# Performance work log

Hardware: AMD Instinct MI355X
Metric: run time of the kernel (lower is better)

Reference implementation:

```python
import jax, jax.numpy as jnp
import numpy as np

B, S, D, K = 32, 512, 512, 2048
NHEADS, NHASH, HLEN = 8, 4, 16
COMMIT = 0.25


def _conv1d(x, w, b):
    # x: [B, C, S], w: [O, I, k] (torch Conv1d layout), 'same' padding for odd k
    k = w.shape[-1]
    y = jax.lax.conv_general_dilated(x, w, (1,), [(k // 2, k // 2)],
                                     dimension_numbers=('NCH', 'OIH', 'NCH'))
    return y + b[None, :, None]


def _mha(x, in_w, in_b, out_w, out_b, nheads):
    # torch nn.MultiheadAttention (batch_first) with packed in_proj
    b, s, d = x.shape
    dh = d // nheads
    qkv = x @ in_w.T + in_b
    q, k, v = jnp.split(qkv, 3, axis=-1)
    sp = lambda t: t.reshape(b, s, nheads, dh).transpose(0, 2, 1, 3)
    q, k, v = sp(q), sp(k), sp(v)
    attn = jax.nn.softmax(jnp.einsum('bhqd,bhkd->bhqk', q, k) * (dh ** -0.5), axis=-1)
    o = jnp.einsum('bhqk,bhkd->bhqd', attn, v).transpose(0, 2, 1, 3).reshape(b, s, d)
    return o @ out_w.T + out_b


def setup_inputs() -> dict:
    key = jax.random.key(0)
    ks = jax.random.split(key, 16)
    w = lambda k, shape, s=0.02: jax.random.normal(k, shape, jnp.float32) * s
    z = lambda *shape: jnp.zeros(shape, jnp.float32)
    return {
        'market_data': jax.random.normal(ks[0], (B, S, D), jnp.float32),
        'W_in': w(ks[1], (D, D)), 'b_in': z(D),
        'pos_enc': w(ks[2], (S, D)),
        'conv3_w': w(ks[3], (D, D, 3)), 'conv3_b': z(D),
        'conv5_w': w(ks[4], (D, D, 5)), 'conv5_b': z(D),
        'conv7_w': w(ks[5], (D, D, 7)), 'conv7_b': z(D),
        'conv9_w': w(ks[6], (D, D, 9)), 'conv9_b': z(D),
        'ms_proj_w': w(ks[7], (D, 4 * D)), 'ms_proj_b': z(D),
        'in_proj_w': w(ks[8], (3 * D, D)), 'in_proj_b': z(3 * D),
        'attn_out_w': w(ks[9], (D, D)), 'attn_out_b': z(D),
        'codebook': jax.random.uniform(ks[10], (K, D), jnp.float32, -1.0 / K, 1.0 / K),
        'hash_w': w(ks[11], (NHASH, HLEN, D), 1.0),
        'reg1_w': w(ks[12], (D // 2, D)), 'reg1_b': z(D // 2),
        'reg2_w': w(ks[13], (K, D // 2)), 'reg2_b': z(K),
    }


def reference(market_data, W_in, b_in, pos_enc, conv3_w, conv3_b, conv5_w, conv5_b,
              conv7_w, conv7_b, conv9_w, conv9_b, ms_proj_w, ms_proj_b,
              in_proj_w, in_proj_b, attn_out_w, attn_out_b, codebook, hash_w,
              reg1_w, reg1_b, reg2_w, reg2_b):
    # input projection
    x = market_data @ W_in.T + b_in                                   # [B,S,D]
    # --- subsequence encoder ---
    xp = x + pos_enc[:x.shape[1]][None]
    xt = xp.transpose(0, 2, 1)                                        # [B,D,S]
    scales = [jax.nn.relu(_conv1d(xt, cw, cb)).transpose(0, 2, 1)
              for cw, cb in ((conv3_w, conv3_b), (conv5_w, conv5_b),
                             (conv7_w, conv7_b), (conv9_w, conv9_b))]
    multi = jnp.concatenate(scales, axis=-1)                          # [B,S,4D]
    proj = multi @ ms_proj_w.T + ms_proj_b                            # [B,S,D]
    enc = proj + _mha(proj, in_proj_w, in_proj_b, attn_out_w, attn_out_b, NHEADS)
    # --- vector quantizer (eval mode: no EMA update) ---
    flat = enc.reshape(-1, D)                                         # [N,D]
    dist = (jnp.sum(flat * flat, axis=1, keepdims=True)
            + jnp.sum(codebook * codebook, axis=1)
            - 2.0 * (flat @ codebook.T))                              # [N,K]
    idx = jnp.argmin(dist, axis=1)                                    # [N]
    quant = codebook[idx].reshape(enc.shape)
    commit = jnp.mean((jax.lax.stop_gradient(quant) - enc) ** 2)
    cb_loss = jnp.mean((quant - jax.lax.stop_gradient(enc)) ** 2)
    vq_loss = COMMIT * commit + cb_loss
    quant_st = enc + jax.lax.stop_gradient(quant - enc)               # straight-through
    # --- hash encoder on semantic ids ---
    hash_codes = (jnp.einsum('bsd,nhd->bsnh', quant_st, hash_w) > 0).astype(jnp.float32)
    # --- regime classifier ---
    h = jax.nn.relu(quant_st @ reg1_w.T + reg1_b)
    regime = jax.nn.softmax(h @ reg2_w.T + reg2_b, axis=-1)
    return (quant_st, vq_loss, idx.reshape(enc.shape[:-1]), hash_codes, regime)
```

## Files before the change

kernel.cpp:

```cpp
#include <hip/hip_runtime.h>
#include <hip/hip_bf16.h>


#define GF_BIAS 1
#define GF_RELU 2
#define GF_ADD  4
#define GF_POS  8
#define GF_ACC  16

typedef _Float16 f16x8 __attribute__((ext_vector_type(8)));
typedef float    f32x4 __attribute__((ext_vector_type(4)));

static constexpr long long O_QUANT = 0LL;
static constexpr long long O_LOSS  = 8388608LL;
static constexpr long long O_IDX   = 8388609LL;
static constexpr long long O_HASH  = 8404993LL;
static constexpr long long O_REG   = 9453569LL;
static constexpr long long O_END   = 43008001LL;

static constexpr long long W_XP    = 0LL;
static constexpr long long W_CT    = 8388608LL;
static constexpr long long W_PROJ  = 16777216LL;
static constexpr long long W_VW    = 25165824LL;
static constexpr long long W_HREG  = 33554432LL;
static constexpr long long W_T     = 34078720LL;
static constexpr long long W_IDX   = 34209792LL;
static constexpr long long W_ASUM  = 34226176LL;
static constexpr long long W_CBB   = 34258944LL;
static constexpr long long W_LPART = 34263040LL;
static constexpr long long W_PBV   = 34271232LL;
static constexpr long long W_PBI   = 34336768LL;
static constexpr long long W_END   = 34402304LL;

__device__ __forceinline__ unsigned int pack_hl(float x)
{
    _Float16 h = (_Float16)x;
    float hf = (float)h;
    _Float16 l = (_Float16)(x - hf);
    unsigned short hb = __builtin_bit_cast(unsigned short, h);
    unsigned short lb = __builtin_bit_cast(unsigned short, l);
    return (unsigned int)hb | ((unsigned int)lb << 16);
}

__device__ __forceinline__ void split2(float x, unsigned short& h, unsigned short& l)
{
    _Float16 hf = (_Float16)x;
    _Float16 lf = (_Float16)(x - (float)hf);
    h = __builtin_bit_cast(unsigned short, hf);
    l = __builtin_bit_cast(unsigned short, lf);
}

__global__ __launch_bounds__(256)
void split_xp_r18(float* __restrict__ xp)
{
    long long i = (long long)blockIdx.x*256 + threadIdx.x;
    float x = xp[i];
    ((unsigned int*)xp)[i] = pack_hl(x);
}

template<int KT>
__global__ __launch_bounds__(256)
void conv_w_tr_r18(const float* __restrict__ w, unsigned int* __restrict__ wt)
{
    long long i = (long long)blockIdx.x*256 + threadIdx.x;
    int o  = (int)(i / (512*KT));
    int rem= (int)(i % (512*KT));
    int t  = rem >> 9;
    int ii = rem & 511;
    wt[i] = pack_hl(w[(long long)o*512*KT + (long long)ii*KT + t]);
}

template<int KT>
__global__ __launch_bounds__(256)
void conv_mfma_r18(const unsigned int* __restrict__ xphl,
                   const unsigned int* __restrict__ wthl,
                   const float* __restrict__ bias, float* __restrict__ outp)
{
    constexpr int PAD = KT / 2;
    __shared__ unsigned short Ah[128][56];
    __shared__ unsigned short Al[128][56];
    __shared__ unsigned short Bh[128][56];
    __shared__ unsigned short Bl[128][56];
    const int tid  = threadIdx.x;
    const int lane = tid & 63;
    const int wave = tid >> 6;
    const int wm = (wave >> 1) * 64, wn = (wave & 1) * 64;
    const int bm = blockIdx.x * 128, bn = blockIdx.y * 128;
    const int l15 = lane & 15;
    const int lk8 = (lane >> 4) * 8;
    const int rbase = (lane >> 4) * 4;
    const int cg   = tid & 7;
    const int rw0  = tid >> 3;

    f32x4 acc[4][4];
    #pragma unroll
    for (int i=0;i<4;i++)
        #pragma unroll
        for (int j=0;j<4;j++)
            acc[i][j] = (f32x4){0.f,0.f,0.f,0.f};

    for (int t = 0; t < KT; ++t) {
        for (int i0 = 0; i0 < 512; i0 += 32) {
            uint4 va[4], vb[4];
            #pragma unroll
            for (int q = 0; q < 4; ++q) {
                const int row = rw0 + q*32;
                const int s   = (bm + row) & 511;
                const int sp  = s + t - PAD;
                if (sp >= 0 && sp < 512)
                    va[q] = *(const uint4*)(xphl + (long long)(bm + row + t - PAD)*512 + i0 + cg*4);
                else
                    va[q] = make_uint4(0u,0u,0u,0u);
                vb[q] = *(const uint4*)(wthl + (long long)(bn + row)*(KT*512) + t*512 + i0 + cg*4);
            }
            __syncthreads();
            #pragma unroll
            for (int q = 0; q < 4; ++q) {
                const int row = rw0 + q*32;
                ushort4 ahi = make_ushort4((unsigned short)(va[q].x & 0xffff),
                                           (unsigned short)(va[q].y & 0xffff),
                                           (unsigned short)(va[q].z & 0xffff),
                                           (unsigned short)(va[q].w & 0xffff));
                ushort4 alo = make_ushort4((unsigned short)(va[q].x >> 16),
                                           (unsigned short)(va[q].y >> 16),
                                           (unsigned short)(va[q].z >> 16),
                                           (unsigned short)(va[q].w >> 16));
                ushort4 bhi = make_ushort4((unsigned short)(vb[q].x & 0xffff),
                                           (unsigned short)(vb[q].y & 0xffff),
                                           (unsigned short)(vb[q].z & 0xffff),
                                           (unsigned short)(vb[q].w & 0xffff));
                ushort4 blo = make_ushort4((unsigned short)(vb[q].x >> 16),
                                           (unsigned short)(vb[q].y >> 16),
                                           (unsigned short)(vb[q].z >> 16),
                                           (unsigned short)(vb[q].w >> 16));
                *(ushort4*)(&Ah[row][cg*4]) = ahi;
                *(ushort4*)(&Al[row][cg*4]) = alo;
                *(ushort4*)(&Bh[row][cg*4]) = bhi;
                *(ushort4*)(&Bl[row][cg*4]) = blo;
            }
            __syncthreads();
            f16x8 ah[4], al[4], bh[4], bl[4];
            #pragma unroll
            for (int mi = 0; mi < 4; ++mi) {
                ah[mi] = *(const f16x8*)(&Ah[wm + mi*16 + l15][lk8]);
                al[mi] = *(const f16x8*)(&Al[wm + mi*16 + l15][lk8]);
            }
            #pragma unroll
            for (int nj = 0; nj < 4; ++nj) {
                bh[nj] = *(const f16x8*)(&Bh[wn + nj*16 + l15][lk8]);
                bl[nj] = *(const f16x8*)(&Bl[wn + nj*16 + l15][lk8]);
            }
            #pragma unroll
            for (int mi = 0; mi < 4; ++mi)
                #pragma unroll
                for (int nj = 0; nj < 4; ++nj) {
                    acc[mi][nj] = __builtin_amdgcn_mfma_f32_16x16x32_f16(ah[mi], bh[nj], acc[mi][nj], 0, 0, 0);
                    acc[mi][nj] = __builtin_amdgcn_mfma_f32_16x16x32_f16(ah[mi], bl[nj], acc[mi][nj], 0, 0, 0);
                    acc[mi][nj] = __builtin_amdgcn_mfma_f32_16x16x32_f16(al[mi], bh[nj], acc[mi][nj], 0, 0, 0);
                }
        }
    }
    #pragma unroll
    for (int mi = 0; mi < 4; ++mi) {
        #pragma unroll
        for (int nj = 0; nj < 4; ++nj) {
            const int col = bn + wn + nj*16 + l15;
            const float bcol = bias[col];
            #pragma unroll
            for (int r = 0; r < 4; ++r) {
                const int row = bm + wm + mi*16 + rbase + r;
                float v = acc[mi][nj][r] + bcol;
                outp[(long long)row*512 + col] = fmaxf(v, 0.0f);
            }
        }
    }
}

template<int FLAGS>
__global__ __launch_bounds__(256)
void gemm_mfma_r18(const float* __restrict__ A, const float* __restrict__ Bm,
                   const float* __restrict__ bias, const float* __restrict__ pos,
                   const float* __restrict__ addsrc, float* __restrict__ C,
                   int Kdim, int lda, int ldb, int ldc)
{
    __shared__ unsigned short Ah[128][56];
    __shared__ unsigned short Al[128][56];
    __shared__ unsigned short Bh[128][56];
    __shared__ unsigned short Bl[128][56];
    const int tid  = threadIdx.x;
    const int lane = tid & 63;
    const int wave = tid >> 6;
    const int wm = (wave >> 1) * 64, wn = (wave & 1) * 64;
    const int bm = blockIdx.x * 128, bn = blockIdx.y * 128;
    const int l15 = lane & 15;
    const int lk8 = (lane >> 4) * 8;
    const int rbase = (lane >> 4) * 4;
    const int cg   = tid & 7;
    const int rw0  = tid >> 3;

    f32x4 acc[4][4];
    #pragma unroll
    for (int i=0;i<4;i++)
        #pragma unroll
        for (int j=0;j<4;j++)
            acc[i][j] = (f32x4){0.f,0.f,0.f,0.f};

    for (int k0 = 0; k0 < Kdim; k0 += 32) {
        float4 fa[4], fb[4];
        #pragma unroll
        for (int q = 0; q < 4; ++q) {
            const int row = rw0 + q*32;
            fa[q] = *(const float4*)(A  + (long long)(bm + row)*lda + k0 + cg*4);
            fb[q] = *(const float4*)(Bm + (long long)(bn + row)*ldb + k0 + cg*4);
        }
        __syncthreads();
        #pragma unroll
        for (int q = 0; q < 4; ++q) {
            const int row = rw0 + q*32;
            ushort4 ah_, al_, bh_, bl_;
            split2(fa[q].x, ah_.x, al_.x);
            split2(fa[q].y, ah_.y, al_.y);
            split2(fa[q].z, ah_.z, al_.z);
            split2(fa[q].w, ah_.w, al_.w);
            split2(fb[q].x, bh_.x, bl_.x);
            split2(fb[q].y, bh_.y, bl_.y);
            split2(fb[q].z, bh_.z, bl_.z);
            split2(fb[q].w, bh_.w, bl_.w);
            *(ushort4*)(&Ah[row][cg*4]) = ah_;
            *(ushort4*)(&Al[row][cg*4]) = al_;
            *(ushort4*)(&Bh[row][cg*4]) = bh_;
            *(ushort4*)(&Bl[row][cg*4]) = bl_;
        }
        __syncthreads();
        f16x8 ah[4], al[4], bh[4], bl[4];
        #pragma unroll
        for (int mi = 0; mi < 4; ++mi) {
            ah[mi] = *(const f16x8*)(&Ah[wm + mi*16 + l15][lk8]);
            al[mi] = *(const f16x8*)(&Al[wm + mi*16 + l15][lk8]);
        }
        #pragma unroll
        for (int nj = 0; nj < 4; ++nj) {
            bh[nj] = *(const f16x8*)(&Bh[wn + nj*16 + l15][lk8]);
            bl[nj] = *(const f16x8*)(&Bl[wn + nj*16 + l15][lk8]);
        }
        #pragma unroll
        for (int mi = 0; mi < 4; ++mi)
            #pragma unroll
            for (int nj = 0; nj < 4; ++nj) {
                acc[mi][nj] = __builtin_amdgcn_mfma_f32_16x16x32_f16(ah[mi], bh[nj], acc[mi][nj], 0, 0, 0);
                acc[mi][nj] = __builtin_amdgcn_mfma_f32_16x16x32_f16(ah[mi], bl[nj], acc[mi][nj], 0, 0, 0);
                acc[mi][nj] = __builtin_amdgcn_mfma_f32_16x16x32_f16(al[mi], bh[nj], acc[mi][nj], 0, 0, 0);
            }
    }
    #pragma unroll
    for (int mi = 0; mi < 4; ++mi) {
        #pragma unroll
        for (int nj = 0; nj < 4; ++nj) {
            const int col = bn + wn + nj*16 + l15;
            #pragma unroll
            for (int r = 0; r < 4; ++r) {
                const int row = bm + wm + mi*16 + rbase + r;
                float v = acc[mi][nj][r];
                if constexpr (FLAGS & GF_BIAS) v += bias[col];
                if constexpr (FLAGS & GF_POS)  v += pos[(long long)(row & 511)*512 + col];
                if constexpr (FLAGS & GF_ADD)  v += addsrc[(long long)row*ldc + col];
                if constexpr (FLAGS & GF_ACC)  v += C[(long long)row*ldc + col];
                if constexpr (FLAGS & GF_RELU) v = fmaxf(v, 0.0f);
                C[(long long)row*ldc + col] = v;
            }
        }
    }
}

__global__ __launch_bounds__(256)
void attn_mfma_r18(const float* __restrict__ Qbuf, const float* __restrict__ Kbuf,
                   const float* __restrict__ Vbuf, float* __restrict__ att)
{
    __shared__ unsigned short Qh[64][68];
    __shared__ unsigned short Ql[64][68];
    __shared__ unsigned short Kh[64][68];
    __shared__ unsigned short Kl[64][68];
    __shared__ unsigned short Vh[64][68];
    __shared__ unsigned short Vl[64][68];
    const int tid  = threadIdx.x;
    const int lane = tid & 63;
    const int wave = tid >> 6;
    const int l15  = lane & 15;
    const int lq   = lane >> 4;
    const int lq8  = lq * 8;
    const int bid = blockIdx.x;
    const int qt = bid & 7, h = (bid >> 3) & 7, b = bid >> 6;
    const int row0 = b*512 + qt*64;

    #pragma unroll
    for (int u = 0; u < 16; ++u) {
        int e = u*256 + tid;
        int r = e >> 6, c = e & 63;
        float q = Qbuf[(long long)(row0 + r)*512 + h*64 + c] * 0.125f;
        unsigned short hs, ls;
        split2(q, hs, ls);
        Qh[r][c] = hs; Ql[r][c] = ls;
    }

    float m[4], l[4];
    f32x4 accO[4];
    #pragma unroll
    for (int r=0;r<4;r++){ m[r] = -1e30f; l[r] = 0.f; }
    #pragma unroll
    for (int j=0;j<4;j++) accO[j] = (f32x4){0.f,0.f,0.f,0.f};

    for (int kv = 0; kv < 512; kv += 64) {
        __syncthreads();
        #pragma unroll
        for (int u = 0; u < 16; ++u) {
            int e = u*256 + tid;
            int r = e >> 6, c = e & 63;
            float kvf = Kbuf[(long long)(b*512 + kv + r)*512 + h*64 + c];
            float vvf = Vbuf[(long long)(b*512 + kv + r)*512 + h*64 + c];
            unsigned short hs, ls;
            split2(kvf, hs, ls);
            Kh[r][c] = hs; Kl[r][c] = ls;
            split2(vvf, hs, ls);
            Vh[c][r] = hs; Vl[c][r] = ls;
        }
        __syncthreads();
        f32x4 accS[4];
        #pragma unroll
        for (int j=0;j<4;j++) accS[j] = (f32x4){0.f,0.f,0.f,0.f};
        #pragma unroll
        for (int ks = 0; ks < 2; ++ks) {
            f16x8 qh = *(const f16x8*)(&Qh[wave*16 + l15][ks*32 + lq8]);
            f16x8 ql = *(const f16x8*)(&Ql[wave*16 + l15][ks*32 + lq8]);
            #pragma unroll
            for (int nj = 0; nj < 4; ++nj) {
                f16x8 kh = *(const f16x8*)(&Kh[nj*16 + l15][ks*32 + lq8]);
                f16x8 kl = *(const f16x8*)(&Kl[nj*16 + l15][ks*32 + lq8]);
                accS[nj] = __builtin_amdgcn_mfma_f32_16x16x32_f16(qh, kh, accS[nj], 0, 0, 0);
                accS[nj] = __builtin_amdgcn_mfma_f32_16x16x32_f16(qh, kl, accS[nj], 0, 0, 0);
                accS[nj] = __builtin_amdgcn_mfma_f32_16x16x32_f16(ql, kh, accS[nj], 0, 0, 0);
            }
        }
        #pragma unroll
        for (int r = 0; r < 4; ++r) {
            float tm = fmaxf(fmaxf(accS[0][r], accS[1][r]), fmaxf(accS[2][r], accS[3][r]));
            #pragma unroll
            for (int msk = 1; msk < 16; msk <<= 1) tm = fmaxf(tm, __shfl_xor(tm, msk, 64));
            float mn = fmaxf(m[r], tm);
            float scale = expf(m[r] - mn);
            float rs = 0.f;
            #pragma unroll
            for (int nj = 0; nj < 4; ++nj) {
                float p = expf(accS[nj][r] - mn);
                accS[nj][r] = p;
                rs += p;
            }
            #pragma unroll
            for (int msk = 1; msk < 16; msk <<= 1) rs += __shfl_xor(rs, msk, 64);
            l[r] = l[r]*scale + rs;
            m[r] = mn;
            #pragma unroll
            for (int nj = 0; nj < 4; ++nj) accO[nj][r] *= scale;
        }
        __syncthreads();
        #pragma unroll
        for (int r = 0; r < 4; ++r)
            #pragma unroll
            for (int nj = 0; nj < 4; ++nj) {
                unsigned short hs, ls;
                split2(accS[nj][r], hs, ls);
                Kh[wave*16 + lq*4 + r][nj*16 + l15] = hs;
                Kl[wave*16 + lq*4 + r][nj*16 + l15] = ls;
            }
        __syncthreads();
        #pragma unroll
        for (int ks = 0; ks < 2; ++ks) {
            f16x8 ph = *(const f16x8*)(&Kh[wave*16 + l15][ks*32 + lq8]);
            f16x8 pl = *(const f16x8*)(&Kl[wave*16 + l15][ks*32 + lq8]);
            #pragma unroll
            for (int nj = 0; nj < 4; ++nj) {
                f16x8 vh = *(const f16x8*)(&Vh[nj*16 + l15][ks*32 + lq8]);
                f16x8 vl = *(const f16x8*)(&Vl[nj*16 + l15][ks*32 + lq8]);
                accO[nj] = __builtin_amdgcn_mfma_f32_16x16x32_f16(ph, vh, accO[nj], 0, 0, 0);
                accO[nj] = __builtin_amdgcn_mfma_f32_16x16x32_f16(ph, vl, accO[nj], 0, 0, 0);
                accO[nj] = __builtin_amdgcn_mfma_f32_16x16x32_f16(pl, vh, accO[nj], 0, 0, 0);
            }
        }
    }
    #pragma unroll
    for (int nj = 0; nj < 4; ++nj)
        #pragma unroll
        for (int r = 0; r < 4; ++r) {
            const int row = row0 + wave*16 + lq*4 + r;
            att[(long long)row*512 + h*64 + nj*16 + l15] = accO[nj][r] / l[r];
        }
}

__global__ __launch_bounds__(256)
void row_sumsq_r18(const float* __restrict__ X, double* __restrict__ outp)
{
    const int row  = blockIdx.x*4 + (threadIdx.x >> 6);
    const int lane = threadIdx.x & 63;
    double s = 0.0;
    #pragma unroll
    for (int u = 0; u < 8; ++u) {
        float v = X[(long long)row*512 + lane + u*64];
        s += (double)v * (double)v;
    }
    #pragma unroll
    for (int msk = 32; msk; msk >>= 1) s += __shfl_xor(s, msk, 64);
    if (lane == 0) outp[row] = s;
}

__global__ __launch_bounds__(256)
void vq_argmin_mfma_r18(const float* __restrict__ enc, const float* __restrict__ cb,
                        const double* __restrict__ Asum, const double* __restrict__ cbB,
                        float* __restrict__ pbv, int* __restrict__ pbi)
{
    __shared__ unsigned int smem[14336];
    unsigned short* AhP = (unsigned short*)smem;
    unsigned short* AlP = AhP + 128*56;
    unsigned short* BhP = AlP + 128*56;
    unsigned short* BlP = BhP + 128*56;
    float* bvsP = (float*)smem;
    int*   bisP = (int*)(smem + 4096);

    const int tid  = threadIdx.x;
    const int lane = tid & 63;
    const int wave = tid >> 6;
    const int wm = (wave >> 1) * 64, wn = (wave & 1) * 64;
    const int bm = blockIdx.x * 128;
    const int l15 = lane & 15;
    const int lk8 = (lane >> 4) * 8;
    const int rbase = (lane >> 4) * 4;
    const int cg   = tid & 7;
    const int rw0  = tid >> 3;

    float bestv[16]; int besti[16];
    #pragma unroll
    for (int g = 0; g < 16; ++g) { bestv[g] = 3.0e38f; besti[g] = 2048; }

    for (int nb = 0; nb < 4; ++nb) {
        const int ct0 = blockIdx.y * 512 + nb * 128;
        f32x4 acc[4][4];
        #pragma unroll
        for (int i=0;i<4;i++)
            #pragma unroll
            for (int j=0;j<4;j++)
                acc[i][j] = (f32x4){0.f,0.f,0.f,0.f};

        for (int k0 = 0; k0 < 512; k0 += 32) {
            float4 fa[4], fb[4];
            #pragma unroll
            for (int q = 0; q < 4; ++q) {
                const int row = rw0 + q*32;
                fa[q] = *(const float4*)(enc + (long long)(bm + row)*512 + k0 + cg*4);
                fb[q] = *(const float4*)(cb  + (long long)(ct0 + row)*512 + k0 + cg*4);
            }
            __syncthreads();
            #pragma unroll
            for (int q = 0; q < 4; ++q) {
                const int row = rw0 + q*32;
                ushort4 ah_, al_, bh_, bl_;
                split2(fa[q].x, ah_.x, al_.x);
                split2(fa[q].y, ah_.y, al_.y);
                split2(fa[q].z, ah_.z, al_.z);
                split2(fa[q].w, ah_.w, al_.w);
                split2(fb[q].x * 2048.0f, bh_.x, bl_.x);
                split2(fb[q].y * 2048.0f, bh_.y, bl_.y);
                split2(fb[q].z * 2048.0f, bh_.z, bl_.z);
                split2(fb[q].w * 2048.0f, bh_.w, bl_.w);
                *(ushort4*)(&AhP[row*56 + cg*4]) = ah_;
                *(ushort4*)(&AlP[row*56 + cg*4]) = al_;
                *(ushort4*)(&BhP[row*56 + cg*4]) = bh_;
                *(ushort4*)(&BlP[row*56 + cg*4]) = bl_;
            }
            __syncthreads();
            f16x8 ah[4], al[4], bh[4], bl[4];
            #pragma unroll
            for (int mi = 0; mi < 4; ++mi) {
                ah[mi] = *(const f16x8*)(&AhP[(wm + mi*16 + l15)*56 + lk8]);
                al[mi] = *(const f16x8*)(&AlP[(wm + mi*16 + l15)*56 + lk8]);
            }
            #pragma unroll
            for (int nj = 0; nj < 4; ++nj) {
                bh[nj] = *(const f16x8*)(&BhP[(wn + nj*16 + l15)*56 + lk8]);
                bl[nj] = *(const f16x8*)(&BlP[(wn + nj*16 + l15)*56 + lk8]);
            }
            #pragma unroll
            for (int mi = 0; mi < 4; ++mi)
                #pragma unroll
                for (int nj = 0; nj < 4; ++nj) {
                    acc[mi][nj] = __builtin_amdgcn_mfma_f32_16x16x32_f16(ah[mi], bh[nj], acc[mi][nj], 0, 0, 0);
                    acc[mi][nj] = __builtin_amdgcn_mfma_f32_16x16x32_f16(ah[mi], bl[nj], acc[mi][nj], 0, 0, 0);
                    acc[mi][nj] = __builtin_amdgcn_mfma_f32_16x16x32_f16(al[mi], bh[nj], acc[mi][nj], 0, 0, 0);
                }
        }
        #pragma unroll
        for (int mi = 0; mi < 4; ++mi) {
            #pragma unroll
            for (int r = 0; r < 4; ++r) {
                const int g = mi*4 + r;
                const float anf = (float)Asum[bm + wm + mi*16 + rbase + r];
                #pragma unroll
                for (int nj = 0; nj < 4; ++nj) {
                    const int col = ct0 + wn + nj*16 + l15;
                    const float bf = (float)cbB[col];
                    const float s1 = anf + bf;
                    const float dot = acc[mi][nj][r] * (1.0f/2048.0f);
                    const float df  = 2.0f * dot;
                    const float qd  = s1 - df;
                    if (qd < bestv[g] || (qd == bestv[g] && col < besti[g])) {
                        bestv[g] = qd; besti[g] = col;
                    }
                }
            }
        }
    }
    __syncthreads();
    #pragma unroll
    for (int mi = 0; mi < 4; ++mi)
        #pragma unroll
        for (int r = 0; r < 4; ++r) {
            const int row  = wm + mi*16 + rbase + r;
            const int slot = (wave & 1)*16 + l15;
            bvsP[row*32 + slot] = bestv[mi*4 + r];
            bisP[row*32 + slot] = besti[mi*4 + r];
        }
    __syncthreads();
    if (tid < 128) {
        float bv = bvsP[tid*32]; int bi = bisP[tid*32];
        #pragma unroll
        for (int s = 1; s < 32; ++s) {
            float v = bvsP[tid*32 + s]; int ii = bisP[tid*32 + s];
            if (v < bv || (v == bv && ii < bi)) { bv = v; bi = ii; }
        }
        pbv[(long long)blockIdx.y*16384 + bm + tid] = bv;
        pbi[(long long)blockIdx.y*16384 + bm + tid] = bi;
    }
}

__global__ __launch_bounds__(256)
void vq_reduce_r18(const float* __restrict__ pbv, const int* __restrict__ pbi,
                   int* __restrict__ idxout)
{
    int n = blockIdx.x*256 + threadIdx.x;
    if (n >= 16384) return;
    float bv = pbv[n]; int bi = pbi[n];
    #pragma unroll
    for (int q = 1; q < 4; ++q) {
        float v = pbv[q*16384 + n]; int ii = pbi[q*16384 + n];
        if (v < bv || (v == bv && ii < bi)) { bv = v; bi = ii; }
    }
    idxout[n] = bi & 2047;
}

__global__ __launch_bounds__(256)
void vq_loss_partial_r18(const float* __restrict__ enc, const float* __restrict__ cb,
                         const int* __restrict__ idxp, double* __restrict__ part)
{
    __shared__ double red[4];
    const int row  = blockIdx.x*4 + (threadIdx.x >> 6);
    const int lane = threadIdx.x & 63;
    const int ci = idxp[row] & 2047;
    double s = 0.0;
    #pragma unroll
    for (int u = 0; u < 8; ++u) {
        int d = lane + u*64;
        double dv = (double)cb[(long long)ci*512 + d] - (double)enc[(long long)row*512 + d];
        s += dv * dv;
    }
    #pragma unroll
    for (int msk = 32; msk; msk >>= 1) s += __shfl_xor(s, msk, 64);
    if (lane == 0) red[threadIdx.x >> 6] = s;
    __syncthreads();
    if (threadIdx.x == 0)
        part[blockIdx.x] = red[0] + red[1] + red[2] + red[3];
}

template<int FLAGS>
__global__ __launch_bounds__(256)
void gemm_bt_r18(const float* __restrict__ A, const float* __restrict__ Bm,
                 const float* __restrict__ bias, const float* __restrict__ pos,
                 const float* __restrict__ addsrc, float* __restrict__ C,
                 int Kdim, int lda, int ldb, int ldc)
{
    __shared__ float As[16][132];
    __shared__ float Bs[16][132];
    const int tid = threadIdx.x;
    const int tx = tid & 15, ty = tid >> 4;
    const int bm = blockIdx.x * 128, bn = blockIdx.y * 128;
    const int r0 = tid >> 2;
    const int kg = (tid & 3) << 2;
    const float* Arow0 = A  + (long long)(bm + r0) * lda + kg;
    const float* Arow1 = A  + (long long)(bm + r0 + 64) * lda + kg;
    const float* Brow0 = Bm + (long long)(bn + r0) * ldb + kg;
    const float* Brow1 = Bm + (long long)(bn + r0 + 64) * ldb + kg;

    float acc[8][8] = {};
    for (int k0 = 0; k0 < Kdim; k0 += 16) {
        float4 a0 = *(const float4*)(Arow0 + k0);
        float4 a1 = *(const float4*)(Arow1 + k0);
        float4 b0 = *(const float4*)(Brow0 + k0);
        float4 b1 = *(const float4*)(Brow1 + k0);
        __syncthreads();
        As[kg+0][r0]=a0.x; As[kg+1][r0]=a0.y; As[kg+2][r0]=a0.z; As[kg+3][r0]=a0.w;
        As[kg+0][r0+64]=a1.x; As[kg+1][r0+64]=a1.y; As[kg+2][r0+64]=a1.z; As[kg+3][r0+64]=a1.w;
        Bs[kg+0][r0]=b0.x; Bs[kg+1][r0]=b0.y; Bs[kg+2][r0]=b0.z; Bs[kg+3][r0]=b0.w;
        Bs[kg+0][r0+64]=b1.x; Bs[kg+1][r0+64]=b1.y; Bs[kg+2][r0+64]=b1.z; Bs[kg+3][r0+64]=b1.w;
        __syncthreads();
        #pragma unroll
        for (int kk = 0; kk < 16; ++kk) {
            float a[8], b[8];
            #pragma unroll
            for (int i=0;i<8;i++) a[i] = As[kk][ty*8+i];
            #pragma unroll
            for (int j=0;j<4;j++) b[j]   = Bs[kk][tx*4+j];
            #pragma unroll
            for (int j=0;j<4;j++) b[4+j] = Bs[kk][64+tx*4+j];
            #pragma unroll
            for (int i=0;i<8;i++)
                #pragma unroll
                for (int j=0;j<8;j++)
                    acc[i][j] = fmaf(a[i], b[j], acc[i][j]);
        }
    }
    #pragma unroll
    for (int i=0;i<8;i++){
        const int row = bm + ty*8 + i;
        #pragma unroll
        for (int j=0;j<8;j++){
            const int col = bn + ((j < 4) ? (tx*4 + j) : (64 + tx*4 + (j-4)));
            float v = acc[i][j];
            if constexpr (FLAGS & GF_BIAS) v += bias[col];
            if constexpr (FLAGS & GF_POS)  v += pos[(long long)(row & 511)*512 + col];
            if constexpr (FLAGS & GF_ADD)  v += addsrc[(long long)row*ldc + col];
            if constexpr (FLAGS & GF_ACC)  v += C[(long long)row*ldc + col];
            if constexpr (FLAGS & GF_RELU) v = fmaxf(v, 0.0f);
            C[(long long)row*ldc + col] = v;
        }
    }
}

__global__ __launch_bounds__(256)
void softmax_rows_r18(float* __restrict__ R)
{
    const int row = blockIdx.x;
    const int tid = threadIdx.x;
    __shared__ float  redf[256];
    __shared__ double redd[256];
    float* p = R + (long long)row * 2048;
    float mx = -1e30f;
    for (int c = tid; c < 2048; c += 256) mx = fmaxf(mx, p[c]);
    redf[tid] = mx; __syncthreads();
    for (int s2 = 128; s2; s2 >>= 1) { if (tid < s2) redf[tid] = fmaxf(redf[tid], redf[tid+s2]); __syncthreads(); }
    mx = redf[0];
    double sum = 0.0;
    for (int c = tid; c < 2048; c += 256) { float e = expf(p[c] - mx); p[c] = e; sum += e; }
    redd[tid] = sum; __syncthreads();
    for (int s2 = 128; s2; s2 >>= 1) { if (tid < s2) redd[tid] += redd[tid+s2]; __syncthreads(); }
    double tot = redd[0];
    for (int c = tid; c < 2048; c += 256) p[c] = (float)((double)p[c] / tot);
}

__global__ __launch_bounds__(256)
void hash_table_r18(const float* __restrict__ cb, const float* __restrict__ hw,
                    float* __restrict__ T)
{
    const int k = blockIdx.x*4 + (threadIdx.x >> 6);
    const int j = threadIdx.x & 63;
    double s = 0.0;
    for (int d = 0; d < 512; ++d)
        s += (double)cb[(long long)k*512 + d] * (double)hw[(long long)j*512 + d];
    T[(long long)k*64 + j] = (s > 0.0) ? 1.0f : 0.0f;
}

__global__ void write_loss_r18(const double* __restrict__ part,
                               float* __restrict__ out)
{
    __shared__ double red[256];
    double s = 0.0;
    for (int i = threadIdx.x; i < 4096; i += 256) s += part[i];
    red[threadIdx.x] = s; __syncthreads();
    for (int s2 = 128; s2; s2 >>= 1) {
        if (threadIdx.x < s2) red[threadIdx.x] += red[threadIdx.x + s2];
        __syncthreads();
    }
    if (threadIdx.x == 0)
        out[O_LOSS] = (float)(1.25 * red[0] / 8388608.0);
}

__global__ __launch_bounds__(256)
void write_regime_r18(const float* __restrict__ R, const int* __restrict__ idxp,
                      float* __restrict__ out)
{
    long long i = (long long)blockIdx.x*256 + threadIdx.x;
    if (i >= 33554432LL) return;
    int n = (int)(i >> 11), c = (int)(i & 2047);
    int ci = idxp[n] & 2047;
    out[O_REG + i] = R[(long long)ci*2048 + c];
}

__global__ __launch_bounds__(256)
void write_hash_r18(const float* __restrict__ T, const int* __restrict__ idxp,
                    float* __restrict__ out)
{
    long long i = (long long)blockIdx.x*256 + threadIdx.x;
    if (i >= 1048576LL) return;
    int n = (int)(i >> 6), j = (int)(i & 63);
    int ci = idxp[n] & 2047;
    out[O_HASH + i] = T[(long long)ci*64 + j];
}

__global__ __launch_bounds__(256)
void write_idx_r18(const int* __restrict__ idxp, float* __restrict__ out)
{
    int n = blockIdx.x*256 + threadIdx.x;
    if (n >= 16384) return;
    out[O_IDX + n] = (float)(idxp[n] & 2047);
}

__global__ __launch_bounds__(256)
void write_quant_r18(const float* __restrict__ cb, const int* __restrict__ idxp,
                     float* __restrict__ out)
{
    long long i = (long long)blockIdx.x*256 + threadIdx.x;
    if (i >= 8388608LL) return;
    int n = (int)(i >> 9), d = (int)(i & 511);
    int ci = idxp[n] & 2047;
    out[O_QUANT + i] = cb[(long long)ci*512 + d];
}

extern "C" void kernel_launch(void* const* d_in, const int* in_sizes, int n_in,
                              void* d_out, int out_size, void* d_ws, size_t ws_size,
                              hipStream_t stream)
{
    (void)in_sizes; (void)n_in; (void)out_size;
    const float* market = (const float*)d_in[0];
    const float* W_in   = (const float*)d_in[1];
    const float* b_in   = (const float*)d_in[2];
    const float* pos    = (const float*)d_in[3];
    const float* c3w = (const float*)d_in[4];  const float* c3b = (const float*)d_in[5];
    const float* c5w = (const float*)d_in[6];  const float* c5b = (const float*)d_in[7];
    const float* c7w = (const float*)d_in[8];  const float* c7b = (const float*)d_in[9];
    const float* c9w = (const float*)d_in[10]; const float* c9b = (const float*)d_in[11];
    const float* msw = (const float*)d_in[12]; const float* msb = (const float*)d_in[13];
    const float* inw = (const float*)d_in[14]; const float* inb = (const float*)d_in[15];
    const float* aow = (const float*)d_in[16]; const float* aob = (const float*)d_in[17];
    const float* cb  = (const float*)d_in[18]; const float* hw  = (const float*)d_in[19];
    const float* r1w = (const float*)d_in[20]; const float* r1b = (const float*)d_in[21];
    const float* r2w = (const float*)d_in[22]; const float* r2b = (const float*)d_in[23];

    if (ws_size < (size_t)W_END * sizeof(float)) return;

    float* ws    = (float*)d_ws;
    float* xp    = ws + W_XP;
    float* convt = ws + W_CT;
    float* projp = ws + W_PROJ;
    unsigned int* wt3 = (unsigned int*)(ws + W_VW);
    unsigned int* wt5 = wt3 + 512*512*3;
    unsigned int* wt7 = wt5 + 512*512*5;
    unsigned int* wt9 = wt7 + 512*512*7;
    float* Vbufp = ws + W_VW;
    float* hregp = ws + W_HREG;
    float* Tp    = ws + W_T;
    int*    idxp  = (int*)(ws + W_IDX);
    double* asump = (double*)(ws + W_ASUM);
    double* cbbp  = (double*)(ws + W_CBB);
    double* lpart = (double*)(ws + W_LPART);
    float*  pbvp  = ws + W_PBV;
    int*    pbip  = (int*)(ws + W_PBI);

    float* out = (float*)d_out;

    float* Qbufp = xp;
    float* attp  = xp;
    float* Kbufp = convt;
    float* encp  = convt;
    float* Rp    = projp;

    const unsigned int* xpu = (const unsigned int*)xp;

    conv_w_tr_r18<3><<<3072, 256, 0, stream>>>(c3w, wt3);
    conv_w_tr_r18<5><<<5120, 256, 0, stream>>>(c5w, wt5);
    conv_w_tr_r18<7><<<7168, 256, 0, stream>>>(c7w, wt7);
    conv_w_tr_r18<9><<<9216, 256, 0, stream>>>(c9w, wt9);

    const dim3 gT(128, 4);

    gemm_mfma_r18<GF_BIAS|GF_POS><<<gT, 256, 0, stream>>>(market, W_in, b_in, pos, nullptr, xp, 512, 512, 512, 512);
    split_xp_r18<<<32768, 256, 0, stream>>>(xp);

    conv_mfma_r18<3><<<gT, 256, 0, stream>>>(xpu, wt3, c3b, convt);
    gemm_mfma_r18<GF_BIAS><<<gT, 256, 0, stream>>>(convt, msw + 0*512, msb, nullptr, nullptr, projp, 512, 512, 2048, 512);
    conv_mfma_r18<5><<<gT, 256, 0, stream>>>(xpu, wt5, c5b, convt);
    gemm_mfma_r18<GF_ACC><<<gT, 256, 0, stream>>>(convt, msw + 1*512, nullptr, nullptr, nullptr, projp, 512, 512, 2048, 512);
    conv_mfma_r18<7><<<gT, 256, 0, stream>>>(xpu, wt7, c7b, convt);
    gemm_mfma_r18<GF_ACC><<<gT, 256, 0, stream>>>(convt, msw + 2*512, nullptr, nullptr, nullptr, projp, 512, 512, 2048, 512);
    conv_mfma_r18<9><<<gT, 256, 0, stream>>>(xpu, wt9, c9b, convt);
    gemm_mfma_r18<GF_ACC><<<gT, 256, 0, stream>>>(convt, msw + 3*512, nullptr, nullptr, nullptr, projp, 512, 512, 2048, 512);

    gemm_mfma_r18<GF_BIAS><<<gT, 256, 0, stream>>>(projp, inw + 512*512,  inb + 512,  nullptr, nullptr, Kbufp, 512, 512, 512, 512);
    gemm_mfma_r18<GF_BIAS><<<gT, 256, 0, stream>>>(projp, inw + 1024*512, inb + 1024, nullptr, nullptr, Vbufp, 512, 512, 512, 512);
    gemm_mfma_r18<GF_BIAS><<<gT, 256, 0, stream>>>(projp, inw,            inb,        nullptr, nullptr, Qbufp, 512, 512, 512, 512);

    attn_mfma_r18<<<2048, 256, 0, stream>>>(Qbufp, Kbufp, Vbufp, attp);

    gemm_mfma_r18<GF_BIAS|GF_ADD><<<gT, 256, 0, stream>>>(attp, aow, aob, nullptr, projp, encp, 512, 512, 512, 512);

    row_sumsq_r18<<<4096, 256, 0, stream>>>(encp, asump);
    row_sumsq_r18<<<512,  256, 0, stream>>>(cb, cbbp);
    vq_argmin_mfma_r18<<<dim3(128, 4), 256, 0, stream>>>(encp, cb, asump, cbbp, pbvp, pbip);
    vq_reduce_r18<<<64, 256, 0, stream>>>(pbvp, pbip, idxp);
    vq_loss_partial_r18<<<4096, 256, 0, stream>>>(encp, cb, idxp, lpart);

    gemm_bt_r18<GF_BIAS|GF_RELU><<<dim3(16, 2),  256, 0, stream>>>(cb, r1w, r1b, nullptr, nullptr, hregp, 512, 512, 512, 256);
    gemm_bt_r18<GF_BIAS><<<dim3(16, 16), 256, 0, stream>>>(hregp, r2w, r2b, nullptr, nullptr, Rp, 256, 256, 256, 2048);
    softmax_rows_r18<<<2048, 256, 0, stream>>>(Rp);
    hash_table_r18<<<512, 256, 0, stream>>>(cb, hw, Tp);

    write_loss_r18<<<1, 256, 0, stream>>>(lpart, out);
    write_regime_r18<<<131072, 256, 0, stream>>>(Rp, idxp, out);
    write_hash_r18<<<4096, 256, 0, stream>>>(Tp, idxp, out);
    write_idx_r18<<<64, 256, 0, stream>>>(idxp, out);
    write_quant_r18<<<32768, 256, 0, stream>>>(cb, idxp, out);
}
```

Baseline: 1.631 ms.

## Reuse haloed input tile across conv taps in MFMA conv kernel

The conv kernel now loops over input-channel chunks on the outside and taps on the inside. For each chunk it loads one 136-row input tile with a 4-row halo into shared memory, then reads it at a shifted row offset per tap instead of reloading the input once per tap. This cuts global reads of the activation by roughly the kernel width and reshapes the LDS tiles to 40-wide rows. In exchange, the weight stores to LDS become scalar 16-bit writes instead of vector writes, and an extra barrier is added per tap. The other kernels are only renamed.

```diff
diff --git a/kernel.cpp b/kernel.cpp
--- a/kernel.cpp
+++ b/kernel.cpp
@@ -51,7 +51,7 @@
 }
 
 __global__ __launch_bounds__(256)
-void split_xp_r18(float* __restrict__ xp)
+void split_xp_r19(float* __restrict__ xp)
 {
     long long i = (long long)blockIdx.x*256 + threadIdx.x;
     float x = xp[i];
@@ -60,7 +60,7 @@
 
 template<int KT>
 __global__ __launch_bounds__(256)
-void conv_w_tr_r18(const float* __restrict__ w, unsigned int* __restrict__ wt)
+void conv_w_tr_r19(const float* __restrict__ w, unsigned int* __restrict__ wt)
 {
     long long i = (long long)blockIdx.x*256 + threadIdx.x;
     int o  = (int)(i / (512*KT));
@@ -72,15 +72,15 @@
 
 template<int KT>
 __global__ __launch_bounds__(256)
-void conv_mfma_r18(const unsigned int* __restrict__ xphl,
+void conv_mfma_r19(const unsigned int* __restrict__ xphl,
                    const unsigned int* __restrict__ wthl,
                    const float* __restrict__ bias, float* __restrict__ outp)
 {
     constexpr int PAD = KT / 2;
-    __shared__ unsigned short Ah[128][56];
-    __shared__ unsigned short Al[128][56];
-    __shared__ unsigned short Bh[128][56];
-    __shared__ unsigned short Bl[128][56];
+    __shared__ unsigned short Ah[136][40];
+    __shared__ unsigned short Al[136][40];
+    __shared__ unsigned short Bh[128][40];
+    __shared__ unsigned short Bl[128][40];
     const int tid  = threadIdx.x;
     const int lane = tid & 63;
     const int wave = tid >> 6;
@@ -89,8 +89,7 @@
     const int l15 = lane & 15;
     const int lk8 = (lane >> 4) * 8;
     const int rbase = (lane >> 4) * 4;
-    const int cg   = tid & 7;
-    const int rw0  = tid >> 3;
+    const int sb = bm & 511;
 
     f32x4 acc[4][4];
     #pragma unroll
@@ -99,51 +98,43 @@
         for (int j=0;j<4;j++)
             acc[i][j] = (f32x4){0.f,0.f,0.f,0.f};
 
-    for (int t = 0; t < KT; ++t) {
-        for (int i0 = 0; i0 < 512; i0 += 32) {
-            uint4 va[4], vb[4];
-            #pragma unroll
-            for (int q = 0; q < 4; ++q) {
-                const int row = rw0 + q*32;
-                const int s   = (bm + row) & 511;
-                const int sp  = s + t - PAD;
-                if (sp >= 0 && sp < 512)
-                    va[q] = *(const uint4*)(xphl + (long long)(bm + row + t - PAD)*512 + i0 + cg*4);
-                else
-                    va[q] = make_uint4(0u,0u,0u,0u);
-                vb[q] = *(const uint4*)(wthl + (long long)(bn + row)*(KT*512) + t*512 + i0 + cg*4);
+    for (int i0 = 0; i0 < 512; i0 += 32) {
+        __syncthreads();
+        for (int sl = tid; sl < 136*8; sl += 256) {
+            const int row = sl >> 3, c = sl & 7;
+            const int srow = sb + row - 4;
+            uint4 v = make_uint4(0u,0u,0u,0u);
+            if (srow >= 0 && srow < 512)
+                v = *(const uint4*)(xphl + (long long)(bm + row - 4)*512 + i0 + c*4);
+            Ah[row][c*4+0] = (unsigned short)(v.x & 0xffff);
+            Ah[row][c*4+1] = (unsigned short)(v.y & 0xffff);
+            Ah[row][c*4+2] = (unsigned short)(v.z & 0xffff);
+            Ah[row][c*4+3] = (unsigned short)(v.w & 0xffff);
+            Al[row][c*4+0] = (unsigned short)(v.x >> 16);
+            Al[row][c*4+1] = (unsigned short)(v.y >> 16);
+            Al[row][c*4+2] = (unsigned short)(v.z >> 16);
+            Al[row][c*4+3] = (unsigned short)(v.w >> 16);
+        }
+        for (int t = 0; t < KT; ++t) {
+            for (int sl = tid; sl < 128*8; sl += 256) {
+                const int row = sl >> 3, c = sl & 7;
+                uint4 v = *(const uint4*)(wthl + (long long)(bn + row)*(KT*512) + t*512 + i0 + c*4);
+                Bh[row][c*4+0] = (unsigned short)(v.x & 0xffff);
+                Bh[row][c*4+1] = (unsigned short)(v.y & 0xffff);
+                Bh[row][c*4+2] = (unsigned short)(v.z & 0xffff);
+                Bh[row][c*4+3] = (unsigned short)(v.w & 0xffff);
+                Bl[row][c*4+0] = (unsigned short)(v.x >> 16);
+                Bl[row][c*4+1] = (unsigned short)(v.y >> 16);
+                Bl[row][c*4+2] = (unsigned short)(v.z >> 16);
+                Bl[row][c*4+3] = (unsigned short)(v.w >> 16);
             }
             __syncthreads();
-            #pragma unroll
-            for (int q = 0; q < 4; ++q) {
-                const int row = rw0 + q*32;
-                ushort4 ahi = make_ushort4((unsigned short)(va[q].x & 0xffff),
-                                           (unsigned short)(va[q].y & 0xffff),
-                                           (unsigned short)(va[q].z & 0xffff),
-                                           (unsigned short)(va[q].w & 0xffff));
-                ushort4 alo = make_ushort4((unsigned short)(va[q].x >> 16),
-                                           (unsigned short)(va[q].y >> 16),
-                                           (unsigned short)(va[q].z >> 16),
-                                           (unsigned short)(va[q].w >> 16));
-                ushort4 bhi = make_ushort4((unsigned short)(vb[q].x & 0xffff),
-                                           (unsigned short)(vb[q].y & 0xffff),
-                                           (unsigned short)(vb[q].z & 0xffff),
-                                           (unsigned short)(vb[q].w & 0xffff));
-                ushort4 blo = make_ushort4((unsigned short)(vb[q].x >> 16),
-                                           (unsigned short)(vb[q].y >> 16),
-                                           (unsigned short)(vb[q].z >> 16),
-                                           (unsigned short)(vb[q].w >> 16));
-                *(ushort4*)(&Ah[row][cg*4]) = ahi;
-                *(ushort4*)(&Al[row][cg*4]) = alo;
-                *(ushort4*)(&Bh[row][cg*4]) = bhi;
-                *(ushort4*)(&Bl[row][cg*4]) = blo;
-            }
-            __syncthreads();
+            const int tofs = t - PAD + 4;
             f16x8 ah[4], al[4], bh[4], bl[4];
             #pragma unroll
             for (int mi = 0; mi < 4; ++mi) {
-                ah[mi] = *(const f16x8*)(&Ah[wm + mi*16 + l15][lk8]);
-                al[mi] = *(const f16x8*)(&Al[wm + mi*16 + l15][lk8]);
+                ah[mi] = *(const f16x8*)(&Ah[wm + mi*16 + l15 + tofs][lk8]);
+                al[mi] = *(const f16x8*)(&Al[wm + mi*16 + l15 + tofs][lk8]);
             }
             #pragma unroll
             for (int nj = 0; nj < 4; ++nj) {
@@ -158,6 +149,7 @@
                     acc[mi][nj] = __builtin_amdgcn_mfma_f32_16x16x32_f16(ah[mi], bl[nj], acc[mi][nj], 0, 0, 0);
                     acc[mi][nj] = __builtin_amdgcn_mfma_f32_16x16x32_f16(al[mi], bh[nj], acc[mi][nj], 0, 0, 0);
                 }
+            if (t + 1 < KT) __syncthreads();
         }
     }
     #pragma unroll
@@ -178,7 +170,7 @@
 
 template<int FLAGS>
 __global__ __launch_bounds__(256)
-void gemm_mfma_r18(const float* __restrict__ A, const float* __restrict__ Bm,
+void gemm_mfma_r19(const float* __restrict__ A, const float* __restrict__ Bm,
                    const float* __restrict__ bias, const float* __restrict__ pos,
                    const float* __restrict__ addsrc, float* __restrict__ C,
                    int Kdim, int lda, int ldb, int ldc)
@@ -273,7 +265,7 @@
 }
 
 __global__ __launch_bounds__(256)
-void attn_mfma_r18(const float* __restrict__ Qbuf, const float* __restrict__ Kbuf,
+void attn_mfma_r19(const float* __restrict__ Qbuf, const float* __restrict__ Kbuf,
                    const float* __restrict__ Vbuf, float* __restrict__ att)
 {
     __shared__ unsigned short Qh[64][68];
@@ -396,7 +388,7 @@
 }
 
 __global__ __launch_bounds__(256)
-void row_sumsq_r18(const float* __restrict__ X, double* __restrict__ outp)
+void row_sumsq_r19(const float* __restrict__ X, double* __restrict__ outp)
 {
     const int row  = blockIdx.x*4 + (threadIdx.x >> 6);
     const int lane = threadIdx.x & 63;
@@ -412,7 +404,7 @@
 }
 
 __global__ __launch_bounds__(256)
-void vq_argmin_mfma_r18(const float* __restrict__ enc, const float* __restrict__ cb,
+void vq_argmin_mfma_r19(const float* __restrict__ enc, const float* __restrict__ cb,
                         const double* __restrict__ Asum, const double* __restrict__ cbB,
                         float* __restrict__ pbv, int* __restrict__ pbi)
 {
@@ -540,7 +532,7 @@
 }
 
 __global__ __launch_bounds__(256)
-void vq_reduce_r18(const float* __restrict__ pbv, const int* __restrict__ pbi,
+void vq_reduce_r19(const float* __restrict__ pbv, const int* __restrict__ pbi,
                    int* __restrict__ idxout)
 {
     int n = blockIdx.x*256 + threadIdx.x;
@@ -555,7 +547,7 @@
 }
 
 __global__ __launch_bounds__(256)
-void vq_loss_partial_r18(const float* __restrict__ enc, const float* __restrict__ cb,
+void vq_loss_partial_r19(const float* __restrict__ enc, const float* __restrict__ cb,
                          const int* __restrict__ idxp, double* __restrict__ part)
 {
     __shared__ double red[4];
@@ -579,7 +571,7 @@
 
 template<int FLAGS>
 __global__ __launch_bounds__(256)
-void gemm_bt_r18(const float* __restrict__ A, const float* __restrict__ Bm,
+void gemm_bt_r19(const float* __restrict__ A, const float* __restrict__ Bm,
                  const float* __restrict__ bias, const float* __restrict__ pos,
                  const float* __restrict__ addsrc, float* __restrict__ C,
                  int Kdim, int lda, int ldb, int ldc)
@@ -642,7 +634,7 @@
 }
 
 __global__ __launch_bounds__(256)
-void softmax_rows_r18(float* __restrict__ R)
+void softmax_rows_r19(float* __restrict__ R)
 {
     const int row = blockIdx.x;
     const int tid = threadIdx.x;
@@ -663,7 +655,7 @@
 }
 
 __global__ __launch_bounds__(256)
-void hash_table_r18(const float* __restrict__ cb, const float* __restrict__ hw,
+void hash_table_r19(const float* __restrict__ cb, const float* __restrict__ hw,
                     float* __restrict__ T)
 {
     const int k = blockIdx.x*4 + (threadIdx.x >> 6);
@@ -674,7 +666,7 @@
     T[(long long)k*64 + j] = (s > 0.0) ? 1.0f : 0.0f;
 }
 
-__global__ void write_loss_r18(const double* __restrict__ part,
+__global__ void write_loss_r19(const double* __restrict__ part,
                                float* __restrict__ out)
 {
     __shared__ double red[256];
@@ -690,7 +682,7 @@
 }
 
 __global__ __launch_bounds__(256)
-void write_regime_r18(const float* __restrict__ R, const int* __restrict__ idxp,
+void write_regime_r19(const float* __restrict__ R, const int* __restrict__ idxp,
                       float* __restrict__ out)
 {
     long long i = (long long)blockIdx.x*256 + threadIdx.x;
@@ -701,7 +693,7 @@
 }
 
 __global__ __launch_bounds__(256)
-void write_hash_r18(const float* __restrict__ T, const int* __restrict__ idxp,
+void write_hash_r19(const float* __restrict__ T, const int* __restrict__ idxp,
                     float* __restrict__ out)
 {
     long long i = (long long)blockIdx.x*256 + threadIdx.x;
@@ -712,7 +704,7 @@
 }
 
 __global__ __launch_bounds__(256)
-void write_idx_r18(const int* __restrict__ idxp, float* __restrict__ out)
+void write_idx_r19(const int* __restrict__ idxp, float* __restrict__ out)
 {
     int n = blockIdx.x*256 + threadIdx.x;
     if (n >= 16384) return;
@@ -720,7 +712,7 @@
 }
 
 __global__ __launch_bounds__(256)
-void write_quant_r18(const float* __restrict__ cb, const int* __restrict__ idxp,
+void write_quant_r19(const float* __restrict__ cb, const int* __restrict__ idxp,
                      float* __restrict__ out)
 {
     long long i = (long long)blockIdx.x*256 + threadIdx.x;
@@ -780,47 +772,47 @@
 
     const unsigned int* xpu = (const unsigned int*)xp;
 
-    conv_w_tr_r18<3><<<3072, 256, 0, stream>>>(c3w, wt3);
-    conv_w_tr_r18<5><<<5120, 256, 0, stream>>>(c5w, wt5);
-    conv_w_tr_r18<7><<<7168, 256, 0, stream>>>(c7w, wt7);
-    conv_w_tr_r18<9><<<9216, 256, 0, stream>>>(c9w, wt9);
+    conv_w_tr_r19<3><<<3072, 256, 0, stream>>>(c3w, wt3);
+    conv_w_tr_r19<5><<<5120, 256, 0, stream>>>(c5w, wt5);
+    conv_w_tr_r19<7><<<7168, 256, 0, stream>>>(c7w, wt7);
+    conv_w_tr_r19<9><<<9216, 256, 0, stream>>>(c9w, wt9);
 
     const dim3 gT(128, 4);
 
-    gemm_mfma_r18<GF_BIAS|GF_POS><<<gT, 256, 0, stream>>>(market, W_in, b_in, pos, nullptr, xp, 512, 512, 512, 512);
-    split_xp_r18<<<32768, 256, 0, stream>>>(xp);
-
-    conv_mfma_r18<3><<<gT, 256, 0, stream>>>(xpu, wt3, c3b, convt);
-    gemm_mfma_r18<GF_BIAS><<<gT, 256, 0, stream>>>(convt, msw + 0*512, msb, nullptr, nullptr, projp, 512, 512, 2048, 512);
-    conv_mfma_r18<5><<<gT, 256, 0, stream>>>(xpu, wt5, c5b, convt);
-    gemm_mfma_r18<GF_ACC><<<gT, 256, 0, stream>>>(convt, msw + 1*512, nullptr, nullptr, nullptr, projp, 512, 512, 2048, 512);
-    conv_mfma_r18<7><<<gT, 256, 0, stream>>>(xpu, wt7, c7b, convt);
-    gemm_mfma_r18<GF_ACC><<<gT, 256, 0, stream>>>(convt, msw + 2*512, nullptr, nullptr, nullptr, projp, 512, 512, 2048, 512);
-    conv_mfma_r18<9><<<gT, 256, 0, stream>>>(xpu, wt9, c9b, convt);
-    gemm_mfma_r18<GF_ACC><<<gT, 256, 0, stream>>>(convt, msw + 3*512, nullptr, nullptr, nullptr, projp, 512, 512, 2048, 512);
-
-    gemm_mfma_r18<GF_BIAS><<<gT, 256, 0, stream>>>(projp, inw + 512*512,  inb + 512,  nullptr, nullptr, Kbufp, 512, 512, 512, 512);
-    gemm_mfma_r18<GF_BIAS><<<gT, 256, 0, stream>>>(projp, inw + 1024*512, inb + 1024, nullptr, nullptr, Vbufp, 512, 512, 512, 512);
-    gemm_mfma_r18<GF_BIAS><<<gT, 256, 0, stream>>>(projp, inw,            inb,        nullptr, nullptr, Qbufp, 512, 512, 512, 512);
-
-    attn_mfma_r18<<<2048, 256, 0, stream>>>(Qbufp, Kbufp, Vbufp, attp);
-
-    gemm_mfma_r18<GF_BIAS|GF_ADD><<<gT, 256, 0, stream>>>(attp, aow, aob, nullptr, projp, encp, 512, 512, 512, 512);
-
-    row_sumsq_r18<<<4096, 256, 0, stream>>>(encp, asump);
-    row_sumsq_r18<<<512,  256, 0, stream>>>(cb, cbbp);
-    vq_argmin_mfma_r18<<<dim3(128, 4), 256, 0, stream>>>(encp, cb, asump, cbbp, pbvp, pbip);
-    vq_reduce_r18<<<64, 256, 0, stream>>>(pbvp, pbip, idxp);
-    vq_loss_partial_r18<<<4096, 256, 0, stream>>>(encp, cb, idxp, lpart);
-
-    gemm_bt_r18<GF_BIAS|GF_RELU><<<dim3(16, 2),  256, 0, stream>>>(cb, r1w, r1b, nullptr, nullptr, hregp, 512, 512, 512, 256);
-    gemm_bt_r18<GF_BIAS><<<dim3(16, 16), 256, 0, stream>>>(hregp, r2w, r2b, nullptr, nullptr, Rp, 256, 256, 256, 2048);
-    softmax_rows_r18<<<2048, 256, 0, stream>>>(Rp);
-    hash_table_r18<<<512, 256, 0, stream>>>(cb, hw, Tp);
-
-    write_loss_r18<<<1, 256, 0, stream>>>(lpart, out);
-    write_regime_r18<<<131072, 256, 0, stream>>>(Rp, idxp, out);
-    write_hash_r18<<<4096, 256, 0, stream>>>(Tp, idxp, out);
-    write_idx_r18<<<64, 256, 0, stream>>>(idxp, out);
-    write_quant_r18<<<32768, 256, 0, stream>>>(cb, idxp, out);
-}
+    gemm_mfma_r19<GF_BIAS|GF_POS><<<gT, 256, 0, stream>>>(market, W_in, b_in, pos, nullptr, xp, 512, 512, 512, 512);
+    split_xp_r19<<<32768, 256, 0, stream>>>(xp);
+
+    conv_mfma_r19<3><<<gT, 256, 0, stream>>>(xpu, wt3, c3b, convt);
+    gemm_mfma_r19<GF_BIAS><<<gT, 256, 0, stream>>>(convt, msw + 0*512, msb, nullptr, nullptr, projp, 512, 512, 2048, 512);
+    conv_mfma_r19<5><<<gT, 256, 0, stream>>>(xpu, wt5, c5b, convt);
+    gemm_mfma_r19<GF_ACC><<<gT, 256, 0, stream>>>(convt, msw + 1*512, nullptr, nullptr, nullptr, projp, 512, 512, 2048, 512);
+    conv_mfma_r19<7><<<gT, 256, 0, stream>>>(xpu, wt7, c7b, convt);
+    gemm_mfma_r19<GF_ACC><<<gT, 256, 0, stream>>>(convt, msw + 2*512, nullptr, nullptr, nullptr, projp, 512, 512, 2048, 512);
+    conv_mfma_r19<9><<<gT, 256, 0, stream>>>(xpu, wt9, c9b, convt);
+    gemm_mfma_r19<GF_ACC><<<gT, 256, 0, stream>>>(convt, msw + 3*512, nullptr, nullptr, nullptr, projp, 512, 512, 2048, 512);
+
+    gemm_mfma_r19<GF_BIAS><<<gT, 256, 0, stream>>>(projp, inw + 512*512,  inb + 512,  nullptr, nullptr, Kbufp, 512, 512, 512, 512);
+    gemm_mfma_r19<GF_BIAS><<<gT, 256, 0, stream>>>(projp, inw + 1024*512, inb + 1024, nullptr, nullptr, Vbufp, 512, 512, 512, 512);
+    gemm_mfma_r19<GF_BIAS><<<gT, 256, 0, stream>>>(projp, inw,            inb,        nullptr, nullptr, Qbufp, 512, 512, 512, 512);
+
+    attn_mfma_r19<<<2048, 256, 0, stream>>>(Qbufp, Kbufp, Vbufp, attp);
+
+    gemm_mfma_r19<GF_BIAS|GF_ADD><<<gT, 256, 0, stream>>>(attp, aow, aob, nullptr, projp, encp, 512, 512, 512, 512);
+
+    row_sumsq_r19<<<4096, 256, 0, stream>>>(encp, asump);
+    row_sumsq_r19<<<512,  256, 0, stream>>>(cb, cbbp);
+    vq_argmin_mfma_r19<<<dim3(128, 4), 256, 0, stream>>>(encp, cb, asump, cbbp, pbvp, pbip);
+    vq_reduce_r19<<<64, 256, 0, stream>>>(pbvp, pbip, idxp);
+    vq_loss_partial_r19<<<4096, 256, 0, stream>>>(encp, cb, idxp, lpart);
+
+    gemm_bt_r19<GF_BIAS|GF_RELU><<<dim3(16, 2),  256, 0, stream>>>(cb, r1w, r1b, nullptr, nullptr, hregp, 512, 512, 512, 256);
+    gemm_bt_r19<GF_BIAS><<<dim3(16, 16), 256, 0, stream>>>(hregp, r2w, r2b, nullptr, nullptr, Rp, 256, 256, 256, 2048);
+    softmax_rows_r19<<<2048, 256, 0, stream>>>(Rp);
+    hash_table_r19<<<512, 256, 0, stream>>>(cb, hw, Tp);
+
+    write_loss_r19<<<1, 256, 0, stream>>>(lpart, out);
+    write_regime_r19<<<131072, 256, 0, stream>>>(Rp, idxp, out);
+    write_hash_r19<<<4096, 256, 0, stream>>>(Tp, idxp, out);
+    write_idx_r19<<<64, 256, 0, stream>>>(idxp, out);
+    write_quant_r19<<<32768, 256, 0, stream>>>(cb, idxp, out);
+}
```

Result: slower. 1.897 ms (+16.3%).
